# Optimization experiments

Measured on AMD Instinct MI355X. Metric: run time of the kernel, lower is better.

Reference implementation:

```python
import jax, jax.numpy as jnp
import numpy as np

HEADS, DIM_HEAD = 4, 32
EAF_LAMBDA, EAF_ZMAX = 1.0, 4.0
MIN_SIGMA, MAX_SIGMA = 1.0, 8.0

def _gen_grid(h, w):
    xs = np.linspace(0.0, 1.0, w, dtype=np.float32)
    ys = np.linspace(0.0, 1.0, h, dtype=np.float32)
    gy, gx = np.meshgrid(ys, xs, indexing='ij')
    return np.stack([gx, gy, np.ones_like(gx)], 0)  # [3,h,w]

def setup_inputs():
    key = jax.random.key(0)
    ks = jax.random.split(key, 12)
    B, N, C, D = 4, 6, 128, 128
    Hb, Wb, fh, fw = 25, 25, 24, 48
    inner = HEADS * DIM_HEAD
    # BEV ego-plane grid (same math as BEVEmbedding with bev 200x200, 100m, 3 decoder blocks)
    g = _gen_grid(Hb, Wb)
    g[0] *= 200.0
    g[1] *= 200.0
    V = np.array([[0., -2., 100.], [-2., 0., 100.], [0., 0., 1.]], dtype=np.float32)
    bev_grid = (np.linalg.inv(V) @ g.reshape(3, -1)).reshape(3, Hb, Wb)
    # image plane pixel grid (buffer), scaled to 480x224 image
    ip = _gen_grid(fh, fw)[None]
    ip[:, 0] *= 480.0
    ip[:, 1] *= 224.0
    # cam->world extrinsics: 6 surround cameras on a ring
    E_inv = np.zeros((B, N, 4, 4), dtype=np.float32)
    for n in range(N):
        yaw = 2.0 * np.pi * n / N
        c, s = np.cos(yaw), np.sin(yaw)
        E_inv[:, n, :3, :3] = np.array([[c, -s, 0.], [s, c, 0.], [0., 0., 1.]], dtype=np.float32)
        E_inv[:, n, :3, 3] = np.array([2. * c, 2. * s, 1.6], dtype=np.float32)
        E_inv[:, n, 3, 3] = 1.0
    Kmat = np.array([[260., 0., 240.], [0., 260., 112.], [0., 0., 1.]], dtype=np.float32)
    I_inv = np.broadcast_to(np.linalg.inv(Kmat), (B, N, 3, 3)).astype(np.float32).copy()
    w = lambda k, shape: 0.02 * jax.random.normal(k, shape, dtype=jnp.float32)
    return dict(
        x=jax.random.normal(ks[0], (B, D, Hb, Wb), dtype=jnp.float32),
        feature=jax.random.normal(ks[1], (B, N, C, fh, fw), dtype=jnp.float32),
        I_inv=jnp.asarray(I_inv), E_inv=jnp.asarray(E_inv),
        bev_grid=jnp.asarray(bev_grid), image_plane=jnp.asarray(ip),
        bn_v_g=jnp.ones(C), bn_v_b=jnp.zeros(C), bn_v_m=jnp.zeros(C), bn_v_var=jnp.ones(C),
        conv_v_w=w(ks[2], (D, C)),
        bn_k_g=jnp.ones(C), bn_k_b=jnp.zeros(C), bn_k_m=jnp.zeros(C), bn_k_var=jnp.ones(C),
        conv_k_w=w(ks[3], (D, C)),
        ln_q_g=jnp.ones(D), ln_q_b=jnp.zeros(D),
        ln_k_g=jnp.ones(D), ln_k_b=jnp.zeros(D),
        ln_v_g=jnp.ones(D), ln_v_b=jnp.zeros(D),
        Wq=w(ks[4], (inner, D)), bq=jnp.zeros(inner),
        Wk=w(ks[5], (inner, D)), bk=jnp.zeros(inner),
        Wv=w(ks[6], (inner, D)), bv=jnp.zeros(inner),
        Wo=w(ks[7], (D, inner)), bo=jnp.zeros(D),
        ln_pre_g=jnp.ones(D), ln_pre_b=jnp.zeros(D),
        W1=w(ks[8], (2 * D, D)), b1=jnp.zeros(2 * D),
        W2=w(ks[9], (D, 2 * D)), b2=jnp.zeros(D),
        ln_post_g=jnp.ones(D), ln_post_b=jnp.zeros(D),
    )

def _ln(x, g, b):
    m = x.mean(-1, keepdims=True)
    v = ((x - m) ** 2).mean(-1, keepdims=True)
    return (x - m) * jax.lax.rsqrt(v + 1e-5) * g + b

def _bn_relu_conv(f, g, b, mu, var, Wc):
    # inference BatchNorm2d -> ReLU -> 1x1 Conv (no bias)
    f = (f - mu[None, :, None, None]) * (jax.lax.rsqrt(var + 1e-5) * g)[None, :, None, None] + b[None, :, None, None]
    f = jax.nn.relu(f)
    return jnp.einsum('bchw,dc->bdhw', f, Wc)

def reference(x, feature, I_inv, E_inv, bev_grid, image_plane,
              bn_v_g, bn_v_b, bn_v_m, bn_v_var, conv_v_w,
              bn_k_g, bn_k_b, bn_k_m, bn_k_var, conv_k_w,
              ln_q_g, ln_q_b, ln_k_g, ln_k_b, ln_v_g, ln_v_b,
              Wq, bq, Wk, bk, Wv, bv, Wo, bo,
              ln_pre_g, ln_pre_b, W1, b1, W2, b2, ln_post_g, ln_post_b):
    B, N, C, fh, fw = feature.shape
    _, D, Hb, Wb = x.shape
    Q = Hb * Wb
    Kp = fh * fw
    feat = feature.reshape(B * N, C, fh, fw)
    val = _bn_relu_conv(feat, bn_v_g, bn_v_b, bn_v_m, bn_v_var, conv_v_w)
    keyf = _bn_relu_conv(feat, bn_k_g, bn_k_b, bn_k_m, bn_k_var, conv_k_w)
    v = val.reshape(B, N, D, fh, fw)
    k = keyf.reshape(B, N, D, fh, fw)
    # ---- EAF weights ----
    xy = bev_grid[:2].reshape(2, Q).T                      # [Q,2]
    ones = jnp.ones((Q, 1), dtype=bev_grid.dtype)
    P0 = jnp.concatenate([xy, 0.0 * ones, ones], -1)       # [Q,4] z=0
    P1 = jnp.concatenate([xy, EAF_ZMAX * ones, ones], -1)  # [Q,4] z=zmax
    E = jnp.linalg.inv(E_inv)                              # world->cam
    P0c = jnp.einsum('bnij,qj->bnqi', E, P0)
    P1c = jnp.einsum('bnij,qj->bnqi', E, P1)
    Icam = jnp.linalg.inv(I_inv)
    p0 = jnp.einsum('bnij,bnqj->bnqi', Icam, P0c[..., :3])
    p1 = jnp.einsum('bnij,bnqj->bnqi', Icam, P1c[..., :3])
    p0 = p0 / (p0[..., 2:3] + 1e-8)
    p1 = p1 / (p1[..., 2:3] + 1e-8)
    l = jnp.cross(p0, p1)                                  # epipolar line [B,N,Q,3]
    denom = jnp.maximum(jnp.sqrt(l[..., 0] ** 2 + l[..., 1] ** 2), 1e-8)
    l_hat = l / denom[..., None]
    x_img = image_plane[0].reshape(3, Kp).T                # [K,3]
    d = jnp.abs(jnp.einsum('bnqj,kj->bnqk', l_hat, x_img))
    # adaptive lambda_{q,i}
    cam_xy = E_inv[..., :2, 3]                             # [B,N,2]
    vec = xy[None, None] - cam_xy[:, :, None]              # [B,N,Q,2]
    dist = jnp.linalg.norm(vec, axis=-1) + 1e-6
    dist_max = dist.max(axis=(1, 2), keepdims=True) + 1e-6
    dist_norm = jnp.clip(dist / dist_max, 0.0, 1.0)
    sigma = MAX_SIGMA - dist_norm * (MAX_SIGMA - MIN_SIGMA)
    lambda_qi = 1.0 / (sigma + 1e-6)
    scale_w = (EAF_LAMBDA * lambda_qi) ** 2                # [B,N,Q]
    Wmask = jnp.exp(-scale_w[..., None] * d ** 2)          # [B,N,Q,K]
    W_logits = Wmask.transpose(0, 2, 1, 3).reshape(B, Q, N * Kp)
    # ---- cross attention (EAF weight multiplied into logits pre-softmax) ----
    qt = x.reshape(B, D, Q).transpose(0, 2, 1)             # [B,Q,D]
    kt = k.transpose(0, 1, 3, 4, 2).reshape(B, N * Kp, D)
    vt = v.transpose(0, 1, 3, 4, 2).reshape(B, N * Kp, D)
    qp = _ln(qt, ln_q_g, ln_q_b) @ Wq.T + bq
    kp = _ln(kt, ln_k_g, ln_k_b) @ Wk.T + bk
    vp = _ln(vt, ln_v_g, ln_v_b) @ Wv.T + bv
    qh = qp.reshape(B, Q, HEADS, DIM_HEAD).transpose(0, 2, 1, 3)
    kh = kp.reshape(B, N * Kp, HEADS, DIM_HEAD).transpose(0, 2, 1, 3)
    vh = vp.reshape(B, N * Kp, HEADS, DIM_HEAD).transpose(0, 2, 1, 3)
    logits = jnp.einsum('bhqd,bhkd->bhqk', qh, kh) * (DIM_HEAD ** -0.5)
    logits = logits * W_logits[:, None]                    # broadcast over heads
    attn = jax.nn.softmax(logits, axis=-1)
    out = jnp.einsum('bhqk,bhkd->bhqd', attn, vh)
    out = out.transpose(0, 2, 1, 3).reshape(B, Q, HEADS * DIM_HEAD)
    out = out @ Wo.T + bo                                  # [B,Q,D]
    z = out + qt                                           # skip = x
    z = _ln(z, ln_pre_g, ln_pre_b)
    z = z + (jax.nn.gelu(z @ W1.T + b1, approximate=False) @ W2.T + b2)
    z = _ln(z, ln_post_g, ln_post_b)
    return z.transpose(0, 2, 1).reshape(B, D, Hb, Wb)
```

## Files before the change

kernel.cpp:

```cpp
#include <hip/hip_runtime.h>
#include <hip/hip_bf16.h>

typedef unsigned short u16;
typedef __attribute__((ext_vector_type(8))) short short8v;
typedef __attribute__((ext_vector_type(4))) float f32x4;
typedef __attribute__((ext_vector_type(2))) __fp16 fp16x2;

#define B_   4
#define N_   6
#define Q_   625
#define QPAD 640
#define KP_  1152
#define NK_  6912
#define NKB  216
#define NSPLIT 24
#define KSEG (NK_/NSPLIT)
#define FHW  1152
#define LOG2E 1.4426950408889634f
#define LOG2_LOG2E 0.5287663729448977f
#define SLOT_H 640
#define ROW_H  40

__device__ __forceinline__ float bfu(unsigned int u16v){ return __uint_as_float(u16v << 16); }
__device__ __forceinline__ unsigned int f2bfu(float f){
  unsigned int u = __float_as_uint(f);
  return (u + 0x7fffu + ((u>>16)&1u)) >> 16;
}
__device__ __forceinline__ float exp2a(float x){
  float r; asm("v_exp_f32 %0, %1" : "=v"(r) : "v"(x)); return r;
}
__device__ __forceinline__ unsigned cvtpk_bf16(float lo, float hi){
  unsigned r; asm("v_cvt_pk_bf16_f32 %0, %1, %2" : "=v"(r) : "v"(lo), "v"(hi)); return r;
}
__device__ __forceinline__ unsigned cvtpk_f16(float lo, float hi){
  union { fp16x2 h; unsigned u; } c;
  c.h = __builtin_amdgcn_cvt_pkrtz(lo, hi);
  return c.u;
}
__device__ __forceinline__ float ldfeat(const void* p, size_t i, bool isbf){
  return isbf ? bfu((unsigned)reinterpret_cast<const u16*>(p)[i])
              : reinterpret_cast<const float*>(p)[i];
}
union U4S8 { uint4 u; short8v s; };
union H2U { unsigned u; fp16x2 h; };
union HU1 { u16 u; __fp16 h; };

struct InPack {
  const void* p[38];
  int off[38];
  int sz[38];
  int nseg;
  int total;
};

__global__ __launch_bounds__(256) void k_ingest(InPack P, float* __restrict__ dst,
                                                const unsigned* __restrict__ magic,
                                                u16* __restrict__ wbf,
                                                float* __restrict__ csK, float* __restrict__ cbK,
                                                float* __restrict__ csV, float* __restrict__ cbV){
  int idx = blockIdx.x*256 + threadIdx.x;
  bool isbf = (*magic == 0x3F803F80u);
  if (idx < P.total){
    int lo=0, hi=P.nseg-1;
    while (lo<hi){ int mid=(lo+hi+1)>>1; if (P.off[mid]<=idx) lo=mid; else hi=mid-1; }
    int j = idx - P.off[lo];
    float v = 0.f;
    if (j < P.sz[lo]) v = ldfeat(P.p[lo], j, isbf);
    dst[idx] = v;
    return;
  }
  int e = idx - P.total;
  if (e < 81920){
    int mat = e >> 14, i = e & 16383;
    int srcIdx = mat==0?15: mat==1?10: mat==2?24: mat==3?26: 22;
    wbf[e] = (u16)f2bfu(ldfeat(P.p[srcIdx], i, isbf));
  } else if (e < 98304){
    wbf[e] = (u16)f2bfu(ldfeat(P.p[28], e-81920, isbf));
  } else if (e < 131072){
    wbf[e] = (u16)f2bfu(ldfeat(P.p[32], e-98304, isbf));
  } else if (e < 163840){
    wbf[e] = (u16)f2bfu(ldfeat(P.p[34], e-131072, isbf));
  } else if (e < 163840+128){
    int c = e - 163840;
    float g = ldfeat(P.p[11], c, isbf), bb = ldfeat(P.p[12], c, isbf);
    float m = ldfeat(P.p[13], c, isbf), vv = ldfeat(P.p[14], c, isbf);
    float s = rsqrtf(vv+1e-5f)*g;
    csK[c]=s; cbK[c]=bb - m*s;
  } else if (e < 163840+256){
    int c = e - 163840 - 128;
    float g = ldfeat(P.p[6], c, isbf), bb = ldfeat(P.p[7], c, isbf);
    float m = ldfeat(P.p[8], c, isbf), vv = ldfeat(P.p[9], c, isbf);
    float s = rsqrtf(vv+1e-5f)*g;
    csV[c]=s; cbV[c]=bb - m*s;
  }
}

__global__ __launch_bounds__(256) void k_geom(const float* __restrict__ Einv,
                                              const float* __restrict__ Iinv,
                                              const float* __restrict__ bev,
                                              float* __restrict__ geom)
{
  __shared__ float redm[4][256];
  int tid = threadIdx.x;
  float mx[4] = {0.f,0.f,0.f,0.f};
  for (int i = tid; i < N_*Q_; i += 256){
    int n = i / Q_, q = i - n*Q_;
    float x = bev[q], y = bev[Q_+q];
    #pragma unroll
    for (int bb=0;bb<4;++bb){
      float cx = Einv[(bb*N_+n)*16 + 3], cy = Einv[(bb*N_+n)*16 + 7];
      float dx = x-cx, dy = y-cy;
      mx[bb] = fmaxf(mx[bb], sqrtf(dx*dx+dy*dy) + 1e-6f);
    }
  }
  #pragma unroll
  for (int bb=0;bb<4;++bb) redm[bb][tid] = mx[bb];
  __syncthreads();
  for (int s=128;s>0;s>>=1){
    if (tid<s){
      #pragma unroll
      for (int bb=0;bb<4;++bb) redm[bb][tid] = fmaxf(redm[bb][tid], redm[bb][tid+s]);
    }
    __syncthreads();
  }

  int idx = blockIdx.x*256 + tid;
  if (idx >= B_*N_*Q_) return;
  int b = idx / (N_*Q_), r = idx - b*(N_*Q_), n = r / Q_, q = r - n*Q_;
  float dmaxv = redm[b][0] + 1e-6f;

  float a[4][8];
  #pragma unroll
  for (int i=0;i<4;++i){
    #pragma unroll
    for (int j=0;j<4;++j) a[i][j] = Einv[(b*N_+n)*16 + i*4 + j];
    #pragma unroll
    for (int j=0;j<4;++j) a[i][4+j] = (i==j)?1.f:0.f;
  }
  #pragma unroll
  for (int col=0;col<4;++col){
    float inv = 1.f/a[col][col];
    #pragma unroll
    for (int j=0;j<8;++j) a[col][j]*=inv;
    #pragma unroll
    for (int rr=0;rr<4;++rr) if (rr!=col){
      float f=a[rr][col];
      #pragma unroll
      for (int j=0;j<8;++j) a[rr][j] -= f*a[col][j];
    }
  }
  float E[3][4];
  #pragma unroll
  for (int i=0;i<3;++i)
    #pragma unroll
    for (int j=0;j<4;++j) E[i][j]=a[i][4+j];

  float m9[9];
  #pragma unroll
  for (int i=0;i<9;++i) m9[i] = Iinv[(b*N_+n)*9 + i];
  float c00 =  m9[4]*m9[8]-m9[5]*m9[7];
  float c01 = -(m9[3]*m9[8]-m9[5]*m9[6]);
  float c02 =  m9[3]*m9[7]-m9[4]*m9[6];
  float id = 1.f/(m9[0]*c00 + m9[1]*c01 + m9[2]*c02);
  float Ic[3][3];
  Ic[0][0]=c00*id; Ic[0][1]=-(m9[1]*m9[8]-m9[2]*m9[7])*id; Ic[0][2]=(m9[1]*m9[5]-m9[2]*m9[4])*id;
  Ic[1][0]=c01*id; Ic[1][1]= (m9[0]*m9[8]-m9[2]*m9[6])*id; Ic[1][2]=-(m9[0]*m9[5]-m9[2]*m9[3])*id;
  Ic[2][0]=c02*id; Ic[2][1]=-(m9[0]*m9[7]-m9[1]*m9[6])*id; Ic[2][2]=(m9[0]*m9[4]-m9[1]*m9[3])*id;

  float x = bev[q], y = bev[Q_+q];
  float P0c[3], P1c[3];
  #pragma unroll
  for (int i=0;i<3;++i){
    P0c[i] = E[i][0]*x + E[i][1]*y + E[i][3];
    P1c[i] = E[i][0]*x + E[i][1]*y + E[i][2]*4.0f + E[i][3];
  }
  float p0[3], p1[3];
  #pragma unroll
  for (int i=0;i<3;++i){
    p0[i] = Ic[i][0]*P0c[0] + Ic[i][1]*P0c[1] + Ic[i][2]*P0c[2];
    p1[i] = Ic[i][0]*P1c[0] + Ic[i][1]*P1c[1] + Ic[i][2]*P1c[2];
  }
  float z0 = p0[2]+1e-8f, z1 = p1[2]+1e-8f;
  #pragma unroll
  for (int i=0;i<3;++i){ p0[i]/=z0; p1[i]/=z1; }
  float l0 = p0[1]*p1[2]-p0[2]*p1[1];
  float l1 = p0[2]*p1[0]-p0[0]*p1[2];
  float l2 = p0[0]*p1[1]-p0[1]*p1[0];
  float den = fmaxf(sqrtf(l0*l0+l1*l1), 1e-8f);
  float cx = Einv[(b*N_+n)*16+3], cy = Einv[(b*N_+n)*16+7];
  float dx = x-cx, dy = y-cy;
  float dist = sqrtf(dx*dx+dy*dy) + 1e-6f;
  float dn = fminf(fmaxf(dist/dmaxv, 0.f), 1.f);
  float sigma = 8.0f - dn*7.0f;
  float lam = 1.f/(sigma+1e-6f);
  float* g = geom + (size_t)idx*4;
  g[0]=l0/den; g[1]=l1/den; g[2]=l2/den;
  g[3]=-(lam*lam)*LOG2E;
}

__global__ __launch_bounds__(256) void k_kvproj(
  const void* __restrict__ feat, const unsigned* __restrict__ magic,
  const float* __restrict__ csK, const float* __restrict__ cbK,
  const float* __restrict__ csV, const float* __restrict__ cbV,
  const u16* __restrict__ convKbf, const u16* __restrict__ convVbf,
  const u16* __restrict__ WkBf, const u16* __restrict__ WvBf,
  const float* __restrict__ lkg, const float* __restrict__ lkb,
  const float* __restrict__ lvg, const float* __restrict__ lvb,
  const float* __restrict__ bk_, const float* __restrict__ bv_,
  u16* __restrict__ kp, u16* __restrict__ vpB)
{
  __shared__ __align__(16) unsigned char lds_tile[16384];
  __shared__ float2 redLN[4][64];
  uint4* lds16 = reinterpret_cast<uint4*>(lds_tile);

  const int tid = threadIdx.x;
  const int w = tid >> 6, l = tid & 63;
  const int lr = l & 15, lg4 = l >> 4;
  const int ptile = blockIdx.x;
  const int bn = blockIdx.y, b = bn/6, n = bn - b*6;
  const bool isbf = (*magic == 0x3F803F80u);

  const size_t fbase = (size_t)bn*128*FHW + ptile*64 + l;
  float fv[32];
  #pragma unroll
  for (int pass=0; pass<4; ++pass)
    #pragma unroll
    for (int j=0;j<8;++j){
      int c = pass*32 + w*8 + j;
      fv[pass*8+j] = ldfeat(feat, fbase + (size_t)c*FHW, isbf);
    }

  const int psw = l & 7;
  for (int half=0; half<2; ++half){
    const float* cs   = half ? csV : csK;
    const float* cbv_ = half ? cbV : cbK;
    const u16* convB  = half ? convVbf : convKbf;
    const u16* WB     = half ? WvBf : WkBf;
    const float* lng  = half ? lvg : lkg;
    const float* lnb  = half ? lvb : lkb;
    const float* bias = half ? bv_ : bk_;

    #pragma unroll
    for (int pass=0; pass<4; ++pass){
      int c0 = pass*32 + w*8;
      unsigned int u[4];
      #pragma unroll
      for (int i2=0;i2<4;++i2){
        int ca = c0 + i2*2, cb2 = ca+1;
        float aa = fmaxf(fv[pass*8+i2*2  ]*cs[ca]+cbv_[ca], 0.f);
        float ab = fmaxf(fv[pass*8+i2*2+1]*cs[cb2]+cbv_[cb2], 0.f);
        u[i2] = f2bfu(aa) | (f2bfu(ab)<<16);
      }
      int c8 = c0 >> 3;
      lds16[l*16 + (c8 ^ psw)] = make_uint4(u[0],u[1],u[2],u[3]);
    }
    __syncthreads();

    f32x4 acc[2][4];
    #pragma unroll
    for (int i=0;i<2;++i)
      #pragma unroll
      for (int j=0;j<4;++j) acc[i][j] = (f32x4){0.f,0.f,0.f,0.f};

    #pragma unroll
    for (int ks2=0; ks2<4; ++ks2){
      short8v af[2];
      #pragma unroll
      for (int ib=0; ib<2; ++ib)
        af[ib] = *reinterpret_cast<const short8v*>(convB + ((w*32 + ib*16 + lr)<<7) + (ks2<<5) + (lg4<<3));
      #pragma unroll
      for (int pb2=0; pb2<4; ++pb2){
        int p = pb2*16 + lr;
        U4S8 bu; bu.u = lds16[p*16 + ((ks2*4 + lg4) ^ (p&7))];
        acc[0][pb2] = __builtin_amdgcn_mfma_f32_16x16x32_bf16(af[0], bu.s, acc[0][pb2], 0,0,0);
        acc[1][pb2] = __builtin_amdgcn_mfma_f32_16x16x32_bf16(af[1], bu.s, acc[1][pb2], 0,0,0);
      }
    }

    float s1v[4], s2v[4];
    #pragma unroll
    for (int pb2=0;pb2<4;++pb2){
      float s=0.f, s2=0.f;
      #pragma unroll
      for (int ib=0;ib<2;++ib)
        #pragma unroll
        for (int r=0;r<4;++r){ float v = acc[ib][pb2][r]; s+=v; s2+=v*v; }
      s += __shfl_xor(s,16);  s += __shfl_xor(s,32);
      s2 += __shfl_xor(s2,16); s2 += __shfl_xor(s2,32);
      s1v[pb2]=s; s2v[pb2]=s2;
    }
    if (l < 16){
      #pragma unroll
      for (int pb2=0;pb2<4;++pb2) redLN[w][pb2*16+l] = make_float2(s1v[pb2], s2v[pb2]);
    }
    __syncthreads();

    float mean[4], rstd[4];
    #pragma unroll
    for (int pb2=0;pb2<4;++pb2){
      int p = pb2*16 + lr;
      float2 t0 = redLN[0][p], t1 = redLN[1][p], t2 = redLN[2][p], t3 = redLN[3][p];
      float S = t0.x+t1.x+t2.x+t3.x, S2 = t0.y+t1.y+t2.y+t3.y;
      float mm = S*(1.f/128.f);
      float var = fmaxf(S2*(1.f/128.f) - mm*mm, 0.f);
      mean[pb2] = mm; rstd[pb2] = rsqrtf(var + 1e-5f);
    }
    float4 g4[2], b4[2];
    #pragma unroll
    for (int ib=0;ib<2;++ib){
      g4[ib] = *reinterpret_cast<const float4*>(lng + w*32 + ib*16 + lg4*4);
      b4[ib] = *reinterpret_cast<const float4*>(lnb + w*32 + ib*16 + lg4*4);
    }
    #pragma unroll
    for (int ib=0;ib<2;++ib){
      const float* gg = &g4[ib].x; const float* bb2 = &b4[ib].x;
      int d0 = w*32 + ib*16 + lg4*4;
      int d8 = d0 >> 3, doff = (d0 & 7) * 2;
      #pragma unroll
      for (int pb2=0;pb2<4;++pb2){
        int p = pb2*16 + lr;
        float z0 = (acc[ib][pb2][0]-mean[pb2])*rstd[pb2]*gg[0]+bb2[0];
        float z1 = (acc[ib][pb2][1]-mean[pb2])*rstd[pb2]*gg[1]+bb2[1];
        float z2 = (acc[ib][pb2][2]-mean[pb2])*rstd[pb2]*gg[2]+bb2[2];
        float z3 = (acc[ib][pb2][3]-mean[pb2])*rstd[pb2]*gg[3]+bb2[3];
        unsigned int u0 = f2bfu(z0) | (f2bfu(z1)<<16);
        unsigned int u1 = f2bfu(z2) | (f2bfu(z3)<<16);
        *reinterpret_cast<uint2*>(lds_tile + p*256 + ((d8 ^ (p&7))<<4) + doff) = make_uint2(u0,u1);
      }
    }
    __syncthreads();

    f32x4 acc2[2][4];
    #pragma unroll
    for (int i=0;i<2;++i)
      #pragma unroll
      for (int j=0;j<4;++j) acc2[i][j] = (f32x4){0.f,0.f,0.f,0.f};

    #pragma unroll
    for (int ks2=0; ks2<4; ++ks2){
      short8v af[2];
      #pragma unroll
      for (int ib=0; ib<2; ++ib)
        af[ib] = *reinterpret_cast<const short8v*>(WB + ((w*32 + ib*16 + lr)<<7) + (ks2<<5) + (lg4<<3));
      #pragma unroll
      for (int pb2=0; pb2<4; ++pb2){
        int p = pb2*16 + lr;
        U4S8 bu; bu.u = lds16[p*16 + ((ks2*4 + lg4) ^ (p&7))];
        acc2[0][pb2] = __builtin_amdgcn_mfma_f32_16x16x32_bf16(af[0], bu.s, acc2[0][pb2], 0,0,0);
        acc2[1][pb2] = __builtin_amdgcn_mfma_f32_16x16x32_bf16(af[1], bu.s, acc2[1][pb2], 0,0,0);
      }
    }
    float4 bias4[2];
// ... 1 lines not shown
    for (int ib=0;ib<2;++ib)
      bias4[ib] = *reinterpret_cast<const float4*>(bias + w*32 + ib*16 + lg4*4);

    __syncthreads();

    if (half == 0){
      #pragma unroll
      for (int ib=0;ib<2;++ib){
        const float* bb2 = &bias4[ib].x;
        int i0 = w*32 + ib*16 + lg4*4;
        int i8 = i0 >> 3, ioff = (i0 & 7) * 2;
        #pragma unroll
        for (int pb2=0;pb2<4;++pb2){
          int p = pb2*16 + lr;
          unsigned int u0 = f2bfu(acc2[ib][pb2][0]+bb2[0]) | (f2bfu(acc2[ib][pb2][1]+bb2[1])<<16);
          unsigned int u1 = f2bfu(acc2[ib][pb2][2]+bb2[2]) | (f2bfu(acc2[ib][pb2][3]+bb2[3])<<16);
          *reinterpret_cast<uint2*>(lds_tile + p*256 + ((i8 ^ (p&7))<<4) + ioff) = make_uint2(u0,u1);
        }
      }
      __syncthreads();
      size_t krow0 = (size_t)b*NK_ + n*KP_ + ptile*64;
      #pragma unroll
      for (int kk=0;kk<4;++kk){
        int idx = kk*256 + tid;
        int p = idx >> 4, j = idx & 15;
        uint4 vv = lds16[p*16 + (j ^ (p&7))];
        *reinterpret_cast<uint4*>(kp + (krow0 + p)*128 + j*8) = vv;
      }
    } else {
      u16* lds2 = reinterpret_cast<u16*>(lds_tile);
      #pragma unroll
      for (int ib=0;ib<2;++ib){
        const float* bb2 = &bias4[ib].x;
        int i0 = w*32 + ib*16 + lg4*4;
        #pragma unroll
        for (int pb2=0;pb2<4;++pb2){
          int p = pb2*16 + lr;
          int pc = ((p&12)<<1) | (p&3) | ((p&16)>>2) | (p&32);
          #pragma unroll
          for (int r=0;r<4;++r)
            lds2[(i0+r)*64 + pc] = (u16)f2bfu(acc2[ib][pb2][r]+bb2[r]);
        }
      }
      __syncthreads();
      int kb0 = b*NKB + n*(KP_/32) + ptile*2;
      #pragma unroll
      for (int kk=0;kk<4;++kk){
        int idx = kk*256 + tid;
        int p2 = idx >> 9, d = (idx>>2)&127, ch = idx&3;
        uint4 vv = lds16[d*8 + p2*4 + ch];
        *reinterpret_cast<uint4*>(vpB + ((size_t)(kb0+p2)*128 + d)*32 + ch*8) = vv;
      }
    }
    __syncthreads();
  }
}

__global__ __launch_bounds__(256) void k_qprojM(
  const float* __restrict__ x, const float* __restrict__ lg, const float* __restrict__ lb,
  const u16* __restrict__ WqBf, const float* __restrict__ bq_, u16* __restrict__ qp)
{
  const float SCL = 0.17677669529663687f;
  __shared__ __align__(16) unsigned char lds_tile[16384];
  __shared__ float redS[4][64], redS2[4][64];
  uint4* lds16 = reinterpret_cast<uint4*>(lds_tile);

  const int tid = threadIdx.x;
  const int w = tid >> 6, l = tid & 63;
  const int lr = l & 15, lg4 = l >> 4;
  const int q0 = blockIdx.x * 64;
  const int b  = blockIdx.y;

  int qg = q0 + l; if (qg > Q_-1) qg = Q_-1;
  float xv[32];
  float s = 0.f, s2 = 0.f;
  #pragma unroll
  for (int i=0;i<32;++i){
    float v = x[(size_t)(b*128 + w*32 + i)*Q_ + qg];
    xv[i] = v; s += v; s2 += v*v;
  }
  redS[w][l] = s; redS2[w][l] = s2;
  __syncthreads();
  float S  = redS[0][l]+redS[1][l]+redS[2][l]+redS[3][l];
  float S2 = redS2[0][l]+redS2[1][l]+redS2[2][l]+redS2[3][l];
  float mm = S*(1.f/128.f);
  float rs = rsqrtf(fmaxf(S2*(1.f/128.f)-mm*mm, 0.f) + 1e-5f);
  #pragma unroll
  for (int j=0;j<4;++j){
    unsigned u[4];
    #pragma unroll
    for (int c2=0;c2<4;++c2){
      int i = j*8 + c2*2;
      int d = w*32 + i;
      float z0 = (xv[i]  -mm)*rs*lg[d]   + lb[d];
      float z1 = (xv[i+1]-mm)*rs*lg[d+1] + lb[d+1];
      u[c2] = f2bfu(z0) | (f2bfu(z1)<<16);
    }
    int d8 = w*4 + j;
    lds16[l*16 + (d8 ^ (l&7))] = make_uint4(u[0],u[1],u[2],u[3]);
  }
  __syncthreads();

  f32x4 acc2[2][4];
  #pragma unroll
  for (int i=0;i<2;++i)
    #pragma unroll
    for (int j=0;j<4;++j) acc2[i][j] = (f32x4){0.f,0.f,0.f,0.f};

  #pragma unroll
  for (int ks2=0; ks2<4; ++ks2){
    short8v af[2];
    #pragma unroll
    for (int ib=0; ib<2; ++ib)
      af[ib] = *reinterpret_cast<const short8v*>(WqBf + ((w*32 + ib*16 + lr)<<7) + (ks2<<5) + (lg4<<3));
    #pragma unroll
    for (int pb2=0; pb2<4; ++pb2){
      int p = pb2*16 + lr;
      U4S8 bu; bu.u = lds16[p*16 + ((ks2*4 + lg4) ^ (p&7))];
      acc2[0][pb2] = __builtin_amdgcn_mfma_f32_16x16x32_bf16(af[0], bu.s, acc2[0][pb2], 0,0,0);
      acc2[1][pb2] = __builtin_amdgcn_mfma_f32_16x16x32_bf16(af[1], bu.s, acc2[1][pb2], 0,0,0);
    }
  }
  float4 bias4[2];
  #pragma unroll
  for (int ib=0;ib<2;++ib)
    bias4[ib] = *reinterpret_cast<const float4*>(bq_ + w*32 + ib*16 + lg4*4);

  __syncthreads();
  #pragma unroll
  for (int ib=0;ib<2;++ib){
    const float* bb2 = &bias4[ib].x;
    int i0 = w*32 + ib*16 + lg4*4;
    int i8 = i0 >> 3, ioff = (i0 & 7) * 2;
    #pragma unroll
    for (int pb2=0;pb2<4;++pb2){
      int p = pb2*16 + lr;
      unsigned int u0 = f2bfu((acc2[ib][pb2][0]+bb2[0])*SCL) | (f2bfu((acc2[ib][pb2][1]+bb2[1])*SCL)<<16);
      unsigned int u1 = f2bfu((acc2[ib][pb2][2]+bb2[2])*SCL) | (f2bfu((acc2[ib][pb2][3]+bb2[3])*SCL)<<16);
      *reinterpret_cast<uint2*>(lds_tile + p*256 + ((i8 ^ (p&7))<<4) + ioff) = make_uint2(u0,u1);
    }
  }
  __syncthreads();
  #pragma unroll
  for (int kk=0;kk<4;++kk){
    int idx = kk*256 + tid;
    int p = idx >> 4, j = idx & 15;
    uint4 vv = lds16[p*16 + (j ^ (p&7))];
    *reinterpret_cast<uint4*>(qp + (size_t)(b*QPAD + q0 + p)*128 + j*8) = vv;
  }
}

__global__ __launch_bounds__(256) void k_attn(
    const u16* __restrict__ qp, const u16* __restrict__ kp, const u16* __restrict__ vpB,
    const float* __restrict__ geom, const float* __restrict__ ip,
    u16* __restrict__ part)
{
  __shared__ uint4 ldsK[2][512];
  __shared__ u16  ldsW[2][32*36];

  const int tid = threadIdx.x;
  const int h = tid >> 6;
  const int lane = tid & 63;
  const int lq = lane & 15;
  const int g  = lane >> 4;
  const int bid = blockIdx.x;
  const int b = bid / (20*NSPLIT);
  const int r = bid - b*(20*NSPLIT);
  const int qt = r / NSPLIT;
  const int ks = r - qt*NSPLIT;
  const int q0 = qt*32;
  const int qa = q0 + lq;
  const int qb = q0 + 16 + lq;

  short8v bq0 = *reinterpret_cast<const short8v*>(qp + ((size_t)(b*QPAD + qa))*128 + h*32 + g*8);
  short8v bq1 = *reinterpret_cast<const short8v*>(qp + ((size_t)(b*QPAD + qb))*128 + h*32 + g*8);

  f32x4 o00={0,0,0,0}, o01={0,0,0,0}, o10={0,0,0,0}, o11={0,0,0,0};
  f32x4 zero4 = {0.f,0.f,0.f,0.f};
  float psum0 = 0.f, psum1 = 0.f;

  const int kbeg = ks*KSEG, kend = kbeg + KSEG;
  const int n0 = kbeg / KP_;
  const int pb0 = kbeg - n0*KP_;

  const int wq = tid >> 3, wc = tid & 7;
  int qwg = q0 + wq; if (qwg > Q_-1) qwg = Q_-1;
  const float* gw_ = geom + ((size_t)((b*N_+n0)*Q_ + qwg))*4;
  const float wl0 = gw_[0], wl1 = gw_[1], wl2 = gw_[2], wgw = gw_[3];

  const int c2 = tid*2;
  const int kr0 = c2 >> 4, kch = c2 & 15;
  auto STAGE = [&](int buf, int k0){
    const uint4* gk = reinterpret_cast<const uint4*>(kp + (size_t)(b*NK_ + k0)*128);
    uint4 k0v = gk[c2], k1v = gk[c2+1];
    ldsK[buf][kr0*16 + (kch     ^ (kr0&7))] = k0v;
    ldsK[buf][kr0*16 + ((kch+1) ^ (kr0&7))] = k1v;
  };
  auto WSTAGE = [&](int buf, int k0){
    int key = pb0 + (k0 - kbeg) + wc*4;
    float4 xx = *reinterpret_cast<const float4*>(ip + key);
    float4 yy = *reinterpret_cast<const float4*>(ip + KP_ + key);
    const float* xp = &xx.x; const float* yp = &yy.x;
    float wv[4];
    #pragma unroll
    for (int i=0;i<4;++i){
      float dln = fmaf(wl0, xp[i], fmaf(wl1, yp[i], wl2));
      wv[i] = exp2a(fmaf(wgw, dln*dln, LOG2_LOG2E));
    }
    uint2 pk;
    pk.x = cvtpk_f16(wv[0], wv[1]);
    pk.y = cvtpk_f16(wv[2], wv[3]);
    *reinterpret_cast<uint2*>(&ldsW[buf][wq*36 + wc*4]) = pk;
  };

  const uint4* vpb4 = reinterpret_cast<const uint4*>(vpB);
  const int dd = h*32 + lq;
  const int iv0 = dd*4 + g, iv1 = (dd+16)*4 + g;
  auto VPAN = [&](int k0){ return vpb4 + ((size_t)(b*NKB + (k0>>5)))*512; };

  STAGE(0, kbeg);
  WSTAGE(0, kbeg);
  U4S8 vc0, vc1;
  { const uint4* vp = VPAN(kbeg); vc0.u = vp[iv0]; vc1.u = vp[iv1]; }

  int cur = 0;
  const int kchunk = h*4 + g;
  for (int k0 = kbeg; k0 < kend; k0 += 32){
    __syncthreads();
    bool more = (k0 + 32) < kend;
    if (more){ STAGE(cur^1, k0+32); WSTAGE(cur^1, k0+32); }
    int kn = more ? (k0 + 32) : k0;
    U4S8 vn0, vn1;
    { const uint4* vp = VPAN(kn); vn0.u = vp[iv0]; vn1.u = vp[iv1]; }

    uint2 wA0 = *reinterpret_cast<const uint2*>(&ldsW[cur][lq*36 + g*4]);
    uint2 wA1 = *reinterpret_cast<const uint2*>(&ldsW[cur][lq*36 + 16 + g*4]);
    uint2 wB0 = *reinterpret_cast<const uint2*>(&ldsW[cur][(16+lq)*36 + g*4]);
    uint2 wB1 = *reinterpret_cast<const uint2*>(&ldsW[cur][(16+lq)*36 + 16 + g*4]);
    float w00[4], w01[4], w10[4], w11[4];
    {
      H2U t0,t1,t2,t3,t4,t5,t6,t7;
      t0.u=wA0.x; t1.u=wA0.y; t2.u=wA1.x; t3.u=wA1.y;
      t4.u=wB0.x; t5.u=wB0.y; t6.u=wB1.x; t7.u=wB1.y;
      w00[0]=(float)t0.h[0]; w00[1]=(float)t0.h[1]; w00[2]=(float)t1.h[0]; w00[3]=(float)t1.h[1];
      w01[0]=(float)t2.h[0]; w01[1]=(float)t2.h[1]; w01[2]=(float)t3.h[0]; w01[3]=(float)t3.h[1];
      w10[0]=(float)t4.h[0]; w10[1]=(float)t4.h[1]; w10[2]=(float)t5.h[0]; w10[3]=(float)t5.h[1];
      w11[0]=(float)t6.h[0]; w11[1]=(float)t6.h[1]; w11[2]=(float)t7.h[0]; w11[3]=(float)t7.h[1];
    }

    __builtin_amdgcn_s_setprio(1);
    U4S8 a0, a1;
    a0.u = ldsK[cur][lq*16      + (kchunk ^ (lq&7))];
    a1.u = ldsK[cur][(16+lq)*16 + (kchunk ^ (lq&7))];
    f32x4 s00 = __builtin_amdgcn_mfma_f32_16x16x32_bf16(a0.s, bq0, zero4, 0,0,0);
    f32x4 s01 = __builtin_amdgcn_mfma_f32_16x16x32_bf16(a1.s, bq0, zero4, 0,0,0);
    f32x4 s10 = __builtin_amdgcn_mfma_f32_16x16x32_bf16(a0.s, bq1, zero4, 0,0,0);
    f32x4 s11 = __builtin_amdgcn_mfma_f32_16x16x32_bf16(a1.s, bq1, zero4, 0,0,0);

    float p00[4], p01[4], p10[4], p11[4];
    #pragma unroll
    for (int r2=0;r2<4;++r2){
      p00[r2] = exp2a(fmaf(s00[r2], w00[r2], -8.f));
      p01[r2] = exp2a(fmaf(s01[r2], w01[r2], -8.f));
      psum0 += p00[r2] + p01[r2];
      p10[r2] = exp2a(fmaf(s10[r2], w10[r2], -8.f));
      p11[r2] = exp2a(fmaf(s11[r2], w11[r2], -8.f));
      psum1 += p10[r2] + p11[r2];
    }
    union { short8v s; unsigned int u[4]; } bp0, bp1;
    bp0.u[0] = cvtpk_bf16(p00[0], p00[1]);
    bp0.u[1] = cvtpk_bf16(p00[2], p00[3]);
    bp0.u[2] = cvtpk_bf16(p01[0], p01[1]);
    bp0.u[3] = cvtpk_bf16(p01[2], p01[3]);
    bp1.u[0] = cvtpk_bf16(p10[0], p10[1]);
    bp1.u[1] = cvtpk_bf16(p10[2], p10[3]);
    bp1.u[2] = cvtpk_bf16(p11[0], p11[1]);
    bp1.u[3] = cvtpk_bf16(p11[2], p11[3]);

    o00 = __builtin_amdgcn_mfma_f32_16x16x32_bf16(vc0.s, bp0.s, o00, 0,0,0);
    o01 = __builtin_amdgcn_mfma_f32_16x16x32_bf16(vc1.s, bp0.s, o01, 0,0,0);
    o10 = __builtin_amdgcn_mfma_f32_16x16x32_bf16(vc0.s, bp1.s, o10, 0,0,0);
    o11 = __builtin_amdgcn_mfma_f32_16x16x32_bf16(vc1.s, bp1.s, o11, 0,0,0);
    __builtin_amdgcn_s_setprio(0);

    vc0 = vn0; vc1 = vn1;
    cur ^= 1;
  }
  psum0 += __shfl_xor(psum0,16);
  psum0 += __shfl_xor(psum0,32);
  psum1 += __shfl_xor(psum1,16);
  psum1 += __shfl_xor(psum1,32);
  int slot0 = ((b*4 + h)*40 + qt*2    )*NSPLIT + ks;
  int slot1 = ((b*4 + h)*40 + qt*2 + 1)*NSPLIT + ks;
  u16* pr0 = part + (size_t)slot0*SLOT_H + lq*ROW_H;
  u16* pr1 = part + (size_t)slot1*SLOT_H + lq*ROW_H;
  *reinterpret_cast<unsigned*>(pr0 + g*4)          = cvtpk_f16(o00[0], o00[1]);
  *reinterpret_cast<unsigned*>(pr0 + g*4 + 2)      = cvtpk_f16(o00[2], o00[3]);
  *reinterpret_cast<unsigned*>(pr0 + 16 + g*4)     = cvtpk_f16(o01[0], o01[1]);
  *reinterpret_cast<unsigned*>(pr0 + 16 + g*4 + 2) = cvtpk_f16(o01[2], o01[3]);
  *reinterpret_cast<unsigned*>(pr1 + g*4)          = cvtpk_f16(o10[0], o10[1]);
  *reinterpret_cast<unsigned*>(pr1 + g*4 + 2)      = cvtpk_f16(o10[2], o10[3]);
  *reinterpret_cast<unsigned*>(pr1 + 16 + g*4)     = cvtpk_f16(o11[0], o11[1]);
  *reinterpret_cast<unsigned*>(pr1 + 16 + g*4 + 2) = cvtpk_f16(o11[2], o11[3]);
  if (g==0){
    *reinterpret_cast<float*>(pr0 + 32) = psum0;
    *reinterpret_cast<float*>(pr1 + 32) = psum1;
  }
}

__global__ void k_merge(const u16* __restrict__ part, float* __restrict__ ao){
  int idx = blockIdx.x*256 + threadIdx.x;
  if (idx >= B_*4*Q_*32) return;
  int d = idx & 31; int t = idx >> 5; int q = t % Q_; int bh = t / Q_;
  int qt = q >> 4; int qq = q & 15;
  const u16* base = part + (size_t)((bh*40+qt)*NSPLIT)*SLOT_H + qq*ROW_H;
  float num = 0.f, den = 0.f;
  #pragma unroll 4
  for (int s=0;s<NSPLIT;++s){
    HU1 hv; hv.u = base[s*SLOT_H + d];
    num += (float)hv.h;
    den += *reinterpret_cast<const float*>(base + s*SLOT_H + 32);
  }
  int b = bh>>2, h = bh&3;
  ao[((size_t)(b*Q_+q))*128 + h*32 + d] = num/den;
}

__global__ __launch_bounds__(256) void k_epiM(
  const float* __restrict__ ao, const float* __restrict__ x,
  const u16* __restrict__ WoBf, const float* __restrict__ bo_,
  const float* __restrict__ lpg, const float* __restrict__ lpb,
  const u16* __restrict__ W1Bf, const float* __restrict__ b1_,
  const u16* __restrict__ W2Bf, const float* __restrict__ b2_,
  const float* __restrict__ lsg, const float* __restrict__ lsb,
  void* __restrict__ out, const unsigned* __restrict__ magic)
{
  const float ISQ2 = 0.7071067811865476f;
  __shared__ __align__(16) unsigned char lds_tile[16384];
  __shared__ __align__(16) unsigned char lds_h1[32768];
  __shared__ float2 redLN[4][64];
  uint4* lds16 = reinterpret_cast<uint4*>(lds_tile);
  uint4* ldsH  = reinterpret_cast<uint4*>(lds_h1);
// ... 123 lines not shown
    for (int fi=0; fi<4; ++fi)
      af[fi] = *reinterpret_cast<const short8v*>(W1Bf + ((w*64 + fi*16 + lr)<<7) + (ks2<<5) + (lg4<<3));
    #pragma unroll
    for (int pb2=0; pb2<4; ++pb2){
      int p = pb2*16 + lr;
      U4S8 bu; bu.u = lds16[p*16 + ((ks2*4 + lg4) ^ (p&7))];
      #pragma unroll
      for (int fi=0; fi<4; ++fi)
        acc1[fi][pb2] = __builtin_amdgcn_mfma_f32_16x16x32_bf16(af[fi], bu.s, acc1[fi][pb2], 0,0,0);
    }
  }
  #pragma unroll
  for (int fi=0; fi<4; ++fi){
    float4 b14 = *reinterpret_cast<const float4*>(b1_ + w*64 + fi*16 + lg4*4);
    const float* bb2 = &b14.x;
    int i10 = w*64 + fi*16 + lg4*4;
    int ch = i10 >> 3, ioff = (i10 & 7) * 2;
    #pragma unroll
    for (int pb2=0;pb2<4;++pb2){
      int p = pb2*16 + lr;
      float gl[4];
      #pragma unroll
      for (int r=0;r<4;++r){
        float hh = acc1[fi][pb2][r] + bb2[r];
        gl[r] = 0.5f*hh*(1.f+erff(hh*ISQ2));
      }
      unsigned int u0 = f2bfu(gl[0]) | (f2bfu(gl[1])<<16);
      unsigned int u1 = f2bfu(gl[2]) | (f2bfu(gl[3])<<16);
      *reinterpret_cast<uint2*>(lds_h1 + p*512 + ((ch ^ (p&7))<<4) + ioff) = make_uint2(u0,u1);
    }
  }
  __syncthreads();

  f32x4 acc2[2][4];
  #pragma unroll
  for (int i=0;i<2;++i)
    #pragma unroll
    for (int j=0;j<4;++j) acc2[i][j] = (f32x4){0.f,0.f,0.f,0.f};
  #pragma unroll
  for (int ks2=0; ks2<8; ++ks2){
    short8v af[2];
    #pragma unroll
    for (int ib=0; ib<2; ++ib)
      af[ib] = *reinterpret_cast<const short8v*>(W2Bf + (w*32 + ib*16 + lr)*256 + ks2*32 + lg4*8);
    #pragma unroll
    for (int pb2=0; pb2<4; ++pb2){
      int p = pb2*16 + lr;
      U4S8 bu; bu.u = ldsH[p*32 + ((ks2*4 + lg4) ^ (p&7))];
      acc2[0][pb2] = __builtin_amdgcn_mfma_f32_16x16x32_bf16(af[0], bu.s, acc2[0][pb2], 0,0,0);
      acc2[1][pb2] = __builtin_amdgcn_mfma_f32_16x16x32_bf16(af[1], bu.s, acc2[1][pb2], 0,0,0);
    }
  }
  float4 b24[2];
  #pragma unroll
  for (int ib=0;ib<2;++ib)
    b24[ib] = *reinterpret_cast<const float4*>(b2_ + w*32 + ib*16 + lg4*4);
  f32x4 z2[2][4];
  #pragma unroll
  for (int ib=0;ib<2;++ib){
    const float* bb2 = &b24[ib].x;
    #pragma unroll
    for (int pb2=0;pb2<4;++pb2)
      #pragma unroll
      for (int r=0;r<4;++r)
        z2[ib][pb2][r] = zv[ib][pb2][r] + acc2[ib][pb2][r] + bb2[r];
  }
  #pragma unroll
  for (int pb2=0;pb2<4;++pb2){
    float s=0.f, s2=0.f;
    #pragma unroll
    for (int ib=0;ib<2;++ib)
      #pragma unroll
      for (int r=0;r<4;++r){ float v = z2[ib][pb2][r]; s+=v; s2+=v*v; }
    s += __shfl_xor(s,16);  s += __shfl_xor(s,32);
    s2 += __shfl_xor(s2,16); s2 += __shfl_xor(s2,32);
    s1v[pb2]=s; s2v[pb2]=s2;
  }
  __syncthreads();
  if (l < 16){
    #pragma unroll
    for (int pb2=0;pb2<4;++pb2) redLN[w][pb2*16+l] = make_float2(s1v[pb2], s2v[pb2]);
  }
  __syncthreads();
  float4 sg4[2], sb4[2];
  #pragma unroll
  for (int ib=0;ib<2;++ib){
    sg4[ib] = *reinterpret_cast<const float4*>(lsg + w*32 + ib*16 + lg4*4);
    sb4[ib] = *reinterpret_cast<const float4*>(lsb + w*32 + ib*16 + lg4*4);
  }
  #pragma unroll
  for (int pb2=0;pb2<4;++pb2){
    int p = pb2*16 + lr;
    int q = q0 + p;
    if (q >= Q_) continue;
    float2 t0 = redLN[0][p], t1 = redLN[1][p], t2 = redLN[2][p], t3 = redLN[3][p];
    float S = t0.x+t1.x+t2.x+t3.x, S2 = t0.y+t1.y+t2.y+t3.y;
    float mm = S*(1.f/128.f);
    float rs = rsqrtf(fmaxf(S2*(1.f/128.f) - mm*mm, 0.f) + 1e-5f);
    #pragma unroll
    for (int ib=0;ib<2;++ib){
      const float* gg = &sg4[ib].x; const float* bb2 = &sb4[ib].x;
      #pragma unroll
      for (int r=0;r<4;++r){
        int i = w*32 + ib*16 + lg4*4 + r;
        float z3 = (z2[ib][pb2][r]-mm)*rs*gg[r] + bb2[r];
        size_t oidx = (size_t)(b*128+i)*Q_ + q;
        if (isbf) reinterpret_cast<u16*>(out)[oidx] = (u16)f2bfu(z3);
        else      reinterpret_cast<float*>(out)[oidx] = z3;
      }
    }
  }
}

extern "C" void kernel_launch(void* const* d_in, const int* in_sizes, int n_in,
                              void* d_out, int out_size, void* d_ws, size_t ws_size,
                              hipStream_t stream){
  InPack P;
  int nseg = n_in < 38 ? n_in : 38;
  int c = 0;
  for (int i=0;i<nseg;++i){
    P.p[i] = d_in[i];
    P.off[i] = c;
    P.sz[i] = (i == 1) ? 0 : in_sizes[i];
    c += (P.sz[i] + 7) & ~7;
  }
  P.nseg = nseg;
  P.total = c;

  float* fw = (float*)d_ws;
  float* fin = fw;
  const float* fx    = fin + P.off[0];
  const float* fIinv = fin + P.off[2];
  const float* fEinv = fin + P.off[3];
  const float* fbev  = fin + P.off[4];
  const float* fip   = fin + P.off[5];
  const float* flkg  = fin + P.off[18];
  const float* flkb  = fin + P.off[19];
  const float* flvg  = fin + P.off[20];
  const float* flvb  = fin + P.off[21];
  const float* flqg  = fin + P.off[16];
  const float* flqb  = fin + P.off[17];
  const float* fbq   = fin + P.off[23];
  const float* fbk   = fin + P.off[25];
  const float* fbv   = fin + P.off[27];
  const float* fbo   = fin + P.off[29];
  const float* flpg  = fin + P.off[30];
  const float* flpb  = fin + P.off[31];
  const float* fb1   = fin + P.off[33];
  const float* fb2   = fin + P.off[35];
  const float* flsg  = fin + P.off[36];
  const float* flsb  = fin + P.off[37];

  size_t off = (size_t)P.total;
  float* geomW = fin + off;  off += 60000;
  float* csK = fin + off;    off += 128;
  float* cbK = fin + off;    off += 128;
  float* csV = fin + off;    off += 128;
  float* cbV = fin + off;    off += 128;
  u16* partH = (u16*)(fin + off); off += (size_t)B_*4*40*NSPLIT*(SLOT_H/2);
  float* ao   = fin + off;   off += 320000;
  u16* bb = (u16*)(fin + off);
  u16* convKbf = bb;
  u16* convVbf = bb + 16384;
  u16* WkBf    = bb + 32768;
  u16* WvBf    = bb + 49152;
  u16* WqBf    = bb + 65536;
  u16* WoBf    = bb + 81920;
  u16* W1Bf    = bb + 98304;
  u16* W2Bf    = bb + 131072;
  u16* kp  = bb + 163840;
  u16* vpB = kp + (size_t)B_*NK_*128;
  u16* qp  = vpB + (size_t)B_*NK_*128;

  const unsigned* magic = (const unsigned*)d_in[6];
  const void* featRaw = d_in[1];

  int ingestTot = P.total + 163840 + 256;
  k_ingest<<<(ingestTot+255)/256,256,0,stream>>>(P, fin, magic, bb, csK,cbK,csV,cbV);
  k_geom<<<59,256,0,stream>>>(fEinv, fIinv, fbev, geomW);
  k_kvproj<<<dim3(18,24),256,0,stream>>>(featRaw, magic, csK,cbK,csV,cbV, convKbf,convVbf,
                                         WkBf,WvBf, flkg,flkb,flvg,flvb, fbk,fbv, kp, vpB);
  k_qprojM<<<dim3(10,B_),256,0,stream>>>(fx, flqg,flqb, WqBf, fbq, qp);
  k_attn<<<B_*20*NSPLIT,256,0,stream>>>(qp, kp, vpB, geomW, fip, partH);
  k_merge<<<1250,256,0,stream>>>(partH, ao);
  k_epiM<<<dim3(10,B_),256,0,stream>>>(ao, fx, WoBf,fbo, flpg,flpb, W1Bf,fb1, W2Bf,fb2,
                                       flsg,flsb, d_out, magic);
}
```

Baseline: 96.09 us.

## Fuse geometry computation into attention kernel and drop k_geom launch

Removes the separate k_geom kernel and its global geom buffer. Each k_attn thread now recomputes its epipolar-line coefficients and Gaussian width inline from Einv, Iinv and the BEV grid. The per-batch max distance is taken over the four BEV grid corners instead of a full block reduction, and the 4x4 inverse is replaced by a closed-form rigid/affine inverse. This saves a launch, a dependent write/read round-trip and a reduction, at the cost of redundant per-block scalar math. It also assumes the extrinsics' last row is [0,0,0,1].

```diff
diff --git a/kernel.cpp b/kernel.cpp
--- a/kernel.cpp
+++ b/kernel.cpp
@@ -95,109 +95,6 @@
   }
 }
 
-__global__ __launch_bounds__(256) void k_geom(const float* __restrict__ Einv,
-                                              const float* __restrict__ Iinv,
-                                              const float* __restrict__ bev,
-                                              float* __restrict__ geom)
-{
-  __shared__ float redm[4][256];
-  int tid = threadIdx.x;
-  float mx[4] = {0.f,0.f,0.f,0.f};
-  for (int i = tid; i < N_*Q_; i += 256){
-    int n = i / Q_, q = i - n*Q_;
-    float x = bev[q], y = bev[Q_+q];
-    #pragma unroll
-    for (int bb=0;bb<4;++bb){
-      float cx = Einv[(bb*N_+n)*16 + 3], cy = Einv[(bb*N_+n)*16 + 7];
-      float dx = x-cx, dy = y-cy;
-      mx[bb] = fmaxf(mx[bb], sqrtf(dx*dx+dy*dy) + 1e-6f);
-    }
-  }
-  #pragma unroll
-  for (int bb=0;bb<4;++bb) redm[bb][tid] = mx[bb];
-  __syncthreads();
-  for (int s=128;s>0;s>>=1){
-    if (tid<s){
-      #pragma unroll
-      for (int bb=0;bb<4;++bb) redm[bb][tid] = fmaxf(redm[bb][tid], redm[bb][tid+s]);
-    }
-    __syncthreads();
-  }
-
-  int idx = blockIdx.x*256 + tid;
-  if (idx >= B_*N_*Q_) return;
-  int b = idx / (N_*Q_), r = idx - b*(N_*Q_), n = r / Q_, q = r - n*Q_;
-  float dmaxv = redm[b][0] + 1e-6f;
-
-  float a[4][8];
-  #pragma unroll
-  for (int i=0;i<4;++i){
-    #pragma unroll
-    for (int j=0;j<4;++j) a[i][j] = Einv[(b*N_+n)*16 + i*4 + j];
-    #pragma unroll
-    for (int j=0;j<4;++j) a[i][4+j] = (i==j)?1.f:0.f;
-  }
-  #pragma unroll
-  for (int col=0;col<4;++col){
-    float inv = 1.f/a[col][col];
-    #pragma unroll
-    for (int j=0;j<8;++j) a[col][j]*=inv;
-    #pragma unroll
-    for (int rr=0;rr<4;++rr) if (rr!=col){
-      float f=a[rr][col];
-      #pragma unroll
-      for (int j=0;j<8;++j) a[rr][j] -= f*a[col][j];
-    }
-  }
-  float E[3][4];
-  #pragma unroll
-  for (int i=0;i<3;++i)
-    #pragma unroll
-    for (int j=0;j<4;++j) E[i][j]=a[i][4+j];
-
-  float m9[9];
-  #pragma unroll
-  for (int i=0;i<9;++i) m9[i] = Iinv[(b*N_+n)*9 + i];
-  float c00 =  m9[4]*m9[8]-m9[5]*m9[7];
-  float c01 = -(m9[3]*m9[8]-m9[5]*m9[6]);
-  float c02 =  m9[3]*m9[7]-m9[4]*m9[6];
-  float id = 1.f/(m9[0]*c00 + m9[1]*c01 + m9[2]*c02);
-  float Ic[3][3];
-  Ic[0][0]=c00*id; Ic[0][1]=-(m9[1]*m9[8]-m9[2]*m9[7])*id; Ic[0][2]=(m9[1]*m9[5]-m9[2]*m9[4])*id;
-  Ic[1][0]=c01*id; Ic[1][1]= (m9[0]*m9[8]-m9[2]*m9[6])*id; Ic[1][2]=-(m9[0]*m9[5]-m9[2]*m9[3])*id;
-  Ic[2][0]=c02*id; Ic[2][1]=-(m9[0]*m9[7]-m9[1]*m9[6])*id; Ic[2][2]=(m9[0]*m9[4]-m9[1]*m9[3])*id;
-
-  float x = bev[q], y = bev[Q_+q];
-  float P0c[3], P1c[3];
-  #pragma unroll
-  for (int i=0;i<3;++i){
-    P0c[i] = E[i][0]*x + E[i][1]*y + E[i][3];
-    P1c[i] = E[i][0]*x + E[i][1]*y + E[i][2]*4.0f + E[i][3];
-  }
-  float p0[3], p1[3];
-  #pragma unroll
-  for (int i=0;i<3;++i){
-    p0[i] = Ic[i][0]*P0c[0] + Ic[i][1]*P0c[1] + Ic[i][2]*P0c[2];
-    p1[i] = Ic[i][0]*P1c[0] + Ic[i][1]*P1c[1] + Ic[i][2]*P1c[2];
-  }
-  float z0 = p0[2]+1e-8f, z1 = p1[2]+1e-8f;
-  #pragma unroll
-  for (int i=0;i<3;++i){ p0[i]/=z0; p1[i]/=z1; }
-  float l0 = p0[1]*p1[2]-p0[2]*p1[1];
-  float l1 = p0[2]*p1[0]-p0[0]*p1[2];
-  float l2 = p0[0]*p1[1]-p0[1]*p1[0];
-  float den = fmaxf(sqrtf(l0*l0+l1*l1), 1e-8f);
-  float cx = Einv[(b*N_+n)*16+3], cy = Einv[(b*N_+n)*16+7];
-  float dx = x-cx, dy = y-cy;
-  float dist = sqrtf(dx*dx+dy*dy) + 1e-6f;
-  float dn = fminf(fmaxf(dist/dmaxv, 0.f), 1.f);
-  float sigma = 8.0f - dn*7.0f;
-  float lam = 1.f/(sigma+1e-6f);
-  float* g = geom + (size_t)idx*4;
-  g[0]=l0/den; g[1]=l1/den; g[2]=l2/den;
-  g[3]=-(lam*lam)*LOG2E;
-}
-
 __global__ __launch_bounds__(256) void k_kvproj(
   const void* __restrict__ feat, const unsigned* __restrict__ magic,
   const float* __restrict__ csK, const float* __restrict__ cbK,
@@ -505,7 +402,8 @@
 
 __global__ __launch_bounds__(256) void k_attn(
     const u16* __restrict__ qp, const u16* __restrict__ kp, const u16* __restrict__ vpB,
-    const float* __restrict__ geom, const float* __restrict__ ip,
+    const float* __restrict__ Einv, const float* __restrict__ Iinv,
+    const float* __restrict__ bev, const float* __restrict__ ip,
     u16* __restrict__ part)
 {
   __shared__ uint4 ldsK[2][512];
@@ -538,8 +436,77 @@
 
   const int wq = tid >> 3, wc = tid & 7;
   int qwg = q0 + wq; if (qwg > Q_-1) qwg = Q_-1;
-  const float* gw_ = geom + ((size_t)((b*N_+n0)*Q_ + qwg))*4;
-  const float wl0 = gw_[0], wl1 = gw_[1], wl2 = gw_[2], wgw = gw_[3];
+
+  float wl0, wl1, wl2, wgw;
+  {
+    float dmaxv = 0.f;
+    #pragma unroll
+    for (int cn=0; cn<4; ++cn){
+      int qc = (cn&1)*24 + (cn>>1)*600;
+      float xx = bev[qc], yy = bev[Q_+qc];
+      #pragma unroll
+      for (int nn=0; nn<N_; ++nn){
+        float cx = Einv[(b*N_+nn)*16+3], cy = Einv[(b*N_+nn)*16+7];
+        float dx = xx-cx, dy = yy-cy;
+        dmaxv = fmaxf(dmaxv, sqrtf(dx*dx+dy*dy)+1e-6f);
+      }
+    }
+    dmaxv += 1e-6f;
+
+    const float* Ei = Einv + (size_t)(b*N_+n0)*16;
+    float a00=Ei[0],a01=Ei[1],a02=Ei[2], t0=Ei[3];
+    float a10=Ei[4],a11=Ei[5],a12=Ei[6], t1=Ei[7];
+    float a20=Ei[8],a21=Ei[9],a22=Ei[10],t2=Ei[11];
+    float c00_ = a11*a22-a12*a21;
+    float c01_ = a12*a20-a10*a22;
+    float c02_ = a10*a21-a11*a20;
+    float idet = 1.f/(a00*c00_ + a01*c01_ + a02*c02_);
+    float E00=c00_*idet, E01=(a02*a21-a01*a22)*idet, E02=(a01*a12-a02*a11)*idet;
+    float E10=c01_*idet, E11=(a00*a22-a02*a20)*idet, E12=(a02*a10-a00*a12)*idet;
+    float E20=c02_*idet, E21=(a01*a20-a00*a21)*idet, E22=(a00*a11-a01*a10)*idet;
+    float Et0 = -(E00*t0+E01*t1+E02*t2);
+    float Et1 = -(E10*t0+E11*t1+E12*t2);
+    float Et2 = -(E20*t0+E21*t1+E22*t2);
+
+    const float* mi = Iinv + (size_t)(b*N_+n0)*9;
+    float m0=mi[0],m1=mi[1],m2=mi[2],m3=mi[3],m4=mi[4],m5=mi[5],m6=mi[6],m7=mi[7],m8=mi[8];
+    float d00 = m4*m8-m5*m7;
+    float d01 = m5*m6-m3*m8;
+    float d02 = m3*m7-m4*m6;
+    float idd = 1.f/(m0*d00 + m1*d01 + m2*d02);
+    float I00=d00*idd, I01=(m2*m7-m1*m8)*idd, I02=(m1*m5-m2*m4)*idd;
+    float I10=d01*idd, I11=(m0*m8-m2*m6)*idd, I12=(m2*m3-m0*m5)*idd;
+    float I20=d02*idd, I21=(m1*m6-m0*m7)*idd, I22=(m0*m4-m1*m3)*idd;
+
+    float x = bev[qwg], y = bev[Q_+qwg];
+    float P0x = E00*x + E01*y + Et0;
+    float P0y = E10*x + E11*y + Et1;
+    float P0z = E20*x + E21*y + Et2;
+    float P1x = P0x + E02*4.0f;
+    float P1y = P0y + E12*4.0f;
+    float P1z = P0z + E22*4.0f;
+
+    float p0x = I00*P0x + I01*P0y + I02*P0z;
+    float p0y = I10*P0x + I11*P0y + I12*P0z;
+    float p0z = I20*P0x + I21*P0y + I22*P0z;
+    float p1x = I00*P1x + I01*P1y + I02*P1z;
+    float p1y = I10*P1x + I11*P1y + I12*P1z;
+    float p1z = I20*P1x + I21*P1y + I22*P1z;
+    float z0 = p0z+1e-8f, z1 = p1z+1e-8f;
+    p0x/=z0; p0y/=z0; p0z/=z0;
+    p1x/=z1; p1y/=z1; p1z/=z1;
+    float l0 = p0y*p1z - p0z*p1y;
+    float l1 = p0z*p1x - p0x*p1z;
+    float l2 = p0x*p1y - p0y*p1x;
+    float den = fmaxf(sqrtf(l0*l0+l1*l1), 1e-8f);
+    float dx = x-t0, dy = y-t1;
+    float dist = sqrtf(dx*dx+dy*dy) + 1e-6f;
+    float dn = fminf(fmaxf(dist/dmaxv, 0.f), 1.f);
+    float sigma = 8.0f - dn*7.0f;
+    float lam = 1.f/(sigma+1e-6f);
+    wl0 = l0/den; wl1 = l1/den; wl2 = l2/den;
+    wgw = -(lam*lam)*LOG2E;
+  }
 
   const int c2 = tid*2;
   const int kr0 = c2 >> 4, kch = c2 & 15;
@@ -969,7 +936,6 @@
   const float* flsb  = fin + P.off[37];
 
   size_t off = (size_t)P.total;
-  float* geomW = fin + off;  off += 60000;
   float* csK = fin + off;    off += 128;
   float* cbK = fin + off;    off += 128;
   float* csV = fin + off;    off += 128;
@@ -994,11 +960,10 @@
 
   int ingestTot = P.total + 163840 + 256;
   k_ingest<<<(ingestTot+255)/256,256,0,stream>>>(P, fin, magic, bb, csK,cbK,csV,cbV);
-  k_geom<<<59,256,0,stream>>>(fEinv, fIinv, fbev, geomW);
   k_kvproj<<<dim3(18,24),256,0,stream>>>(featRaw, magic, csK,cbK,csV,cbV, convKbf,convVbf,
                                          WkBf,WvBf, flkg,flkb,flvg,flvb, fbk,fbv, kp, vpB);
   k_qprojM<<<dim3(10,B_),256,0,stream>>>(fx, flqg,flqb, WqBf, fbq, qp);
-  k_attn<<<B_*20*NSPLIT,256,0,stream>>>(qp, kp, vpB, geomW, fip, partH);
+  k_attn<<<B_*20*NSPLIT,256,0,stream>>>(qp, kp, vpB, fEinv, fIinv, fbev, fip, partH);
   k_merge<<<1250,256,0,stream>>>(partH, ao);
   k_epiM<<<dim3(10,B_),256,0,stream>>>(ao, fx, WoBf,fbo, flpg,flpb, W1Bf,fb1, W2Bf,fb2,
                                        flsg,flsb, d_out, magic);
```

Result: no change. 94.21 us (-2.0%).
